# Kernel optimization log

Measured on AMD Instinct MI355X. Metric: run time of the kernel, lower is better.

Reference implementation:

```python
import jax, jax.numpy as jnp
import numpy as np
import math

HID = 128      # hidden_dim == d_inner (expand=1)
NSTATE = 8     # d_state
K = 4          # scan directions
RANK = math.ceil(HID / 16)  # dt_rank = 8
B, H, W = 4, 64, 64


def _ln(x, g, b, eps=1e-5):
    m = jnp.mean(x, -1, keepdims=True)
    v = jnp.mean((x - m) ** 2, -1, keepdims=True)
    return (x - m) * jax.lax.rsqrt(v + eps) * g + b


def _ss2d(x, in_w, conv_w, conv_b, xproj_w, dt_w, dt_b, A_logs, Ds, ln_g, ln_b, out_w):
    # x: [B,H,W,C] -> VMamba SS2D with d_inner=C, 4-direction selective scan
    Bn, Hh, Ww, C = x.shape
    D, L = C, Hh * Ww
    N = A_logs.shape[-1]
    R = dt_w.shape[-1]
    xz = x @ in_w.T                      # [B,H,W,2D]
    xc, z = jnp.split(xz, 2, axis=-1)
    xc = xc.transpose(0, 3, 1, 2)        # [B,D,H,W]
    xc = jax.lax.conv_general_dilated(xc, conv_w, (1, 1), 'SAME', feature_group_count=D)
    xc = jax.nn.silu(xc + conv_b[None, :, None, None])
    x_hw = xc.reshape(Bn, D, L)
    x_wh = xc.transpose(0, 1, 3, 2).reshape(Bn, D, L)
    xs = jnp.stack([x_hw, x_wh, x_hw[..., ::-1], x_wh[..., ::-1]], 1)  # [B,K,D,L]
    x_dbl = jnp.einsum('bkdl,kcd->bkcl', xs, xproj_w)
    dts, Bs, Cs = x_dbl[:, :, :R], x_dbl[:, :, R:R + N], x_dbl[:, :, R + N:]
    dt = jax.nn.softplus(jnp.einsum('bkrl,kdr->bkdl', dts, dt_w) + dt_b[None, :, :, None])
    A = -jnp.exp(A_logs.reshape(K, D, N))  # [K,D,N]

    def step(h, inp):
        x_t, dt_t, B_t, C_t = inp          # [B,K,D],[B,K,D],[B,K,N],[B,K,N]
        h = h * jnp.exp(dt_t[..., None] * A) + dt_t[..., None] * B_t[:, :, None, :] * x_t[..., None]
        return h, jnp.einsum('bkdn,bkn->bkd', h, C_t)

    h0 = jnp.zeros((Bn, K, D, N), x.dtype)
    _, ys = jax.lax.scan(step, h0, (xs.transpose(3, 0, 1, 2), dt.transpose(3, 0, 1, 2),
                                    Bs.transpose(3, 0, 1, 2), Cs.transpose(3, 0, 1, 2)))
    out_y = ys.transpose(1, 2, 3, 0) + Ds.reshape(K, D)[None, :, :, None] * xs  # [B,K,D,L]
    wh_y = out_y[:, 3, :, ::-1].reshape(Bn, D, Ww, Hh).transpose(0, 1, 3, 2).reshape(Bn, D, L)
    invwh_y = out_y[:, 1].reshape(Bn, D, Ww, Hh).transpose(0, 1, 3, 2).reshape(Bn, D, L)
    y = out_y[:, 0] + out_y[:, 2, :, ::-1] + wh_y + invwh_y
    y = _ln(y.transpose(0, 2, 1).reshape(Bn, Hh, Ww, D), ln_g, ln_b)
    return (y * jax.nn.silu(z)) @ out_w.T


def _enhance(x, g, b, w, bias):
    return jax.nn.gelu(_ln(x, g, b) @ w.T + bias, approximate=False)


def setup_inputs() -> dict:
    key = jax.random.key(0)
    ks = jax.random.split(key, 12)
    f = lambda k, s, sc=0.02: jax.random.normal(k, s, jnp.float32) * sc
    return dict(
        sar_feat=jax.random.normal(ks[0], (B, H, W, HID), jnp.float32),
        opt_feat=jax.random.normal(ks[1], (B, H, W, HID), jnp.float32),
        ss_in_w=f(ks[2], (2, 2 * HID, HID)),
        ss_conv_w=f(ks[3], (2, HID, 1, 3, 3), 0.1),
        ss_conv_b=f(ks[4], (2, HID)),
        ss_xproj_w=f(ks[5], (2, K, RANK + 2 * NSTATE, HID)),
        ss_dt_w=f(ks[6], (2, K, HID, RANK), 0.1),
        ss_dt_b=f(ks[7], (2, K, HID), 0.1),
        ss_Alogs=jnp.tile(jnp.log(jnp.arange(1, NSTATE + 1, dtype=jnp.float32)), (2, K * HID, 1)),
        ss_Ds=jnp.ones((2, K * HID), jnp.float32),
        ss_ln_g=jnp.ones((2, HID), jnp.float32),
        ss_ln_b=jnp.zeros((2, HID), jnp.float32),
        ss_out_w=f(ks[8], (2, HID, HID)),
        enh_ln_g=jnp.ones((2, HID), jnp.float32),
        enh_ln_b=jnp.zeros((2, HID), jnp.float32),
        enh_w=f(ks[9], (2, HID, HID)),
        enh_b=jnp.zeros((2, HID), jnp.float32),
    )


def reference(sar_feat, opt_feat, ss_in_w, ss_conv_w, ss_conv_b, ss_xproj_w, ss_dt_w,
              ss_dt_b, ss_Alogs, ss_Ds, ss_ln_g, ss_ln_b, ss_out_w,
              enh_ln_g, enh_ln_b, enh_w, enh_b):
    # cat([opt,sar],-1)[...,:C] == opt ; cat([sar,opt],-1)[...,:C] == sar (faithful identity slice)
    # index 0 = cross_ss2d_s2o (input opt), index 1 = cross_ss2d_o2s (input sar)
    xin = jnp.stack([opt_feat, sar_feat])
    guided = jax.vmap(_ss2d)(xin, ss_in_w, ss_conv_w, ss_conv_b, ss_xproj_w, ss_dt_w,
                             ss_dt_b, ss_Alogs, ss_Ds, ss_ln_g, ss_ln_b, ss_out_w)
    # enhance params: index 0 = enhance_sar (on sar_guided=guided[1]), index 1 = enhance_opt (on opt_guided=guided[0])
    enh_in = jnp.stack([guided[1], guided[0]])
    enhanced = jax.vmap(_enhance)(enh_in, enh_ln_g, enh_ln_b, enh_w, enh_b)
    return (sar_feat + enhanced[0], opt_feat + enhanced[1])
```

## Files before the change

### kernel.cpp

```cpp
#include <hip/hip_runtime.h>
#include <hip/hip_bf16.h>
#include <math.h>

#define DEV __device__ __forceinline__

static constexpr int LL = 4096;
static constexpr int DD = 128;
static constexpr int SEG = 64;
static constexpr float LOG2E = 1.4426950408889634f;
static constexpr float LN2 = 0.6931471805599453f;

DEV float silu_(float x) { return x / (1.f + __expf(-x)); }
DEV float erf_(float x) {
  const float ax = fabsf(x);
  const float t = 1.f / fmaf(0.3275911f, ax, 1.f);
  float p = fmaf(1.061405429f, t, -1.453152027f);
  p = fmaf(p, t, 1.421413741f);
  p = fmaf(p, t, -0.284496736f);
  p = fmaf(p, t, 0.254829592f);
  p = p * t;
  const float r = 1.f - p * __expf(-ax * ax);
  return x < 0.f ? -r : r;
}
DEV float gelu_(float x) { return 0.5f * x * (1.f + erf_(x * 0.7071067811865475f)); }
DEV float sp_(float x) {
  const float t = __builtin_amdgcn_exp2f(-fabsf(x) * LOG2E);
  return fmaxf(x, 0.f) + LN2 * __builtin_amdgcn_logf(1.f + t);
}

template <int CTRL>
DEV float dpp_add_(float x) {
  int y = __builtin_amdgcn_update_dpp(0, __float_as_int(x), CTRL, 0xF, 0xF, true);
  return x + __int_as_float(y);
}

DEV void seg_base_step(int k, int s, int& base, int& step) {
  if (k == 0)      { base = s * 64;        step = 1;   }
  else if (k == 1) { base = s;             step = 64;  }
  else if (k == 2) { base = 4095 - s * 64; step = -1;  }
  else             { base = 4095 - s;      step = -64; }
}

__global__ __launch_bounds__(256) void k_inproj(
    const float* __restrict__ sar, const float* __restrict__ opt,
    const float* __restrict__ in_w, float* __restrict__ xz) {
  const int lt = blockIdx.x, ct = blockIdx.y, mb = blockIdx.z;
  const int m = mb >> 2;
  const float* __restrict__ x = (m == 0 ? opt : sar) + (size_t)(mb & 3) * (LL * DD);
  const float* __restrict__ W = in_w + (size_t)m * 256 * DD;
  __shared__ float sA[64][68];
  __shared__ float sW[64][68];
  const int tid = threadIdx.x;
  const int tc = tid & 15, tl = tid >> 4;
  float acc[4][4] = {};
  for (int db = 0; db < 2; ++db) {
    __syncthreads();
    for (int idx = tid; idx < 64 * 16; idx += 256) {
      const int r = idx >> 4, d4 = (idx & 15) << 2;
      *(float4*)&sA[r][d4] = *(const float4*)&x[(size_t)(lt * 64 + r) * DD + db * 64 + d4];
      *(float4*)&sW[r][d4] = *(const float4*)&W[(size_t)(ct * 64 + r) * DD + db * 64 + d4];
    }
    __syncthreads();
#pragma unroll 4
    for (int d = 0; d < 64; d += 4) {
      float4 a[4], w[4];
#pragma unroll
      for (int q = 0; q < 4; ++q) a[q] = *(const float4*)&sA[tl * 4 + q][d];
#pragma unroll
      for (int j = 0; j < 4; ++j) w[j] = *(const float4*)&sW[tc + 16 * j][d];
#pragma unroll
      for (int j = 0; j < 4; ++j)
#pragma unroll
        for (int q = 0; q < 4; ++q)
          acc[j][q] += a[q].x * w[j].x + a[q].y * w[j].y + a[q].z * w[j].z + a[q].w * w[j].w;
    }
  }
  float* __restrict__ dst = xz + ((size_t)mb * 256 + ct * 64) * LL + lt * 64;
#pragma unroll
  for (int j = 0; j < 4; ++j) {
    float4 v = make_float4(acc[j][0], acc[j][1], acc[j][2], acc[j][3]);
    *(float4*)&dst[(size_t)(tc + 16 * j) * LL + tl * 4] = v;
  }
}

__global__ __launch_bounds__(256) void k_conv(
    const float* __restrict__ xz, const float* __restrict__ conv_w,
    const float* __restrict__ conv_b, float* __restrict__ xc) {
  const int ht = blockIdx.x, dg = blockIdx.y, mb = blockIdx.z;
  const int m = mb >> 2;
  __shared__ float sIn[8][18][66];
  __shared__ float sOut[1024][8];
  const float* __restrict__ src = xz + ((size_t)mb * 256 + dg * 8) * LL;
  const int tid = threadIdx.x;
  for (int idx = tid; idx < 8 * 18 * 66; idx += 256) {
    const int dd = idx / (18 * 66);
    const int rem = idx - dd * (18 * 66);
    const int hh = rem / 66, ww = rem - hh * 66;
    const int h = ht * 16 + hh - 1, w = ww - 1;
    float v = 0.f;
    if (h >= 0 && h < 64 && w >= 0 && w < 64) v = src[(size_t)dd * LL + h * 64 + w];
    sIn[dd][hh][ww] = v;
  }
  __syncthreads();
  const int dd = tid & 7, wv = tid >> 3;
  const int dch = dg * 8 + dd;
  float wk[9];
#pragma unroll
  for (int t = 0; t < 9; ++t) wk[t] = conv_w[((size_t)m * DD + dch) * 9 + t];
  const float bias = conv_b[m * DD + dch];
  for (int hh = 0; hh < 16; ++hh) {
#pragma unroll
    for (int wh = 0; wh < 2; ++wh) {
      const int w = wv + wh * 32;
      float s = bias;
#pragma unroll
      for (int kh = 0; kh < 3; ++kh)
#pragma unroll
        for (int kw = 0; kw < 3; ++kw)
          s = fmaf(sIn[dd][hh + kh][w + kw], wk[kh * 3 + kw], s);
      sOut[hh * 64 + w][dd] = silu_(s);
    }
  }
  __syncthreads();
  float* __restrict__ dst = xc + (size_t)mb * LL * DD + dg * 8;
#pragma unroll
  for (int r = 0; r < 4; ++r) {
    const int pos = tid + r * 256;
    const int l = ht * 1024 + pos;
    *(float4*)&dst[(size_t)l * DD + 0] = *(const float4*)&sOut[pos][0];
    *(float4*)&dst[(size_t)l * DD + 4] = *(const float4*)&sOut[pos][4];
  }
}

__global__ __launch_bounds__(256) void k_xproj(
    const float* __restrict__ xc, const float* __restrict__ xproj_w,
    float* __restrict__ xdbl) {
  const int lt = blockIdx.x, k = blockIdx.y, mb = blockIdx.z;
  const int m = mb >> 2, mbk = mb * 4 + k;
  __shared__ float sX[64][132];
  __shared__ float sW[24][132];
  const int tid = threadIdx.x;
  const float* __restrict__ src = xc + (size_t)mb * LL * DD;
  int base, step;
  seg_base_step(k, lt, base, step);
  for (int idx = tid; idx < 64 * 32; idx += 256) {
    const int l = idx >> 5, d4 = (idx & 31) << 2;
    *(float4*)&sX[l][d4] = *(const float4*)&src[(size_t)(base + l * step) * DD + d4];
  }
  const float* __restrict__ Wsrc = xproj_w + ((size_t)m * 4 + k) * 24 * DD;
  for (int idx = tid; idx < 24 * 32; idx += 256) {
    const int r = idx >> 5, d4 = (idx & 31) << 2;
    *(float4*)&sW[r][d4] = *(const float4*)&Wsrc[(size_t)r * DD + d4];
  }
  __syncthreads();
  const int l = tid >> 2, cg = tid & 3;
  float acc[6] = {};
#pragma unroll 8
  for (int d = 0; d < 128; d += 4) {
    const float4 xv = *(const float4*)&sX[l][d];
#pragma unroll
    for (int j = 0; j < 6; ++j) {
      const float4 wv = *(const float4*)&sW[cg * 6 + j][d];
      acc[j] += xv.x * wv.x + xv.y * wv.y + xv.z * wv.z + xv.w * wv.w;
    }
  }
  float* __restrict__ dst = xdbl + ((size_t)mbk * LL + lt * 64 + l) * 24 + cg * 6;
#pragma unroll
  for (int j = 0; j < 6; ++j) dst[j] = acc[j];
}


template <bool REV, bool FAST>
DEV void scan1_dir(const float* __restrict__ slds, const float* __restrict__ xs0,
                   ptrdiff_t sstep, const float* __restrict__ aln2,
                   const float* __restrict__ wreg, float bw,
                   float* __restrict__ h, float& dtsum) {
  float xreg[8];
#pragma unroll
  for (int t = 0; t < 8; ++t)
    xreg[t] = xs0[(ptrdiff_t)(REV ? 63 - t : t) * sstep];
#pragma unroll 8
  for (int j = 0; j < 64; ++j) {
    const float x = xreg[j & 7];
    if (j + 8 < 64) xreg[j & 7] = xs0[(ptrdiff_t)(REV ? 55 - j : j + 8) * sstep];
    const float4 t0 = *(const float4*)&slds[j * 24 + 0];
    const float4 t1 = *(const float4*)&slds[j * 24 + 4];
    float s = bw;
    s = fmaf(t0.x, wreg[0], s); s = fmaf(t0.y, wreg[1], s);
    s = fmaf(t0.z, wreg[2], s); s = fmaf(t0.w, wreg[3], s);
    s = fmaf(t1.x, wreg[4], s); s = fmaf(t1.y, wreg[5], s);
    s = fmaf(t1.z, wreg[6], s); s = fmaf(t1.w, wreg[7], s);
    const float dt = sp_(s);
    const float u = dt * x;
    dtsum += dt;
    float q1, q2, q3, q4, q5, q6, q7, q8;
    if constexpr (FAST) {
      q1 = __builtin_amdgcn_exp2f(dt * aln2[0]);
      q2 = q1 * q1; q3 = q2 * q1; q4 = q2 * q2;
      q5 = q4 * q1; q6 = q4 * q2; q7 = q4 * q3; q8 = q4 * q4;
    } else {
      q1 = __builtin_amdgcn_exp2f(dt * aln2[0]);
      q2 = __builtin_amdgcn_exp2f(dt * aln2[1]);
      q3 = __builtin_amdgcn_exp2f(dt * aln2[2]);
      q4 = __builtin_amdgcn_exp2f(dt * aln2[3]);
      q5 = __builtin_amdgcn_exp2f(dt * aln2[4]);
      q6 = __builtin_amdgcn_exp2f(dt * aln2[5]);
      q7 = __builtin_amdgcn_exp2f(dt * aln2[6]);
      q8 = __builtin_amdgcn_exp2f(dt * aln2[7]);
    }
    const float4 b0 = *(const float4*)&slds[j * 24 + 8];
    const float4 b1 = *(const float4*)&slds[j * 24 + 12];
    h[0] = fmaf(h[0], q1, u * b0.x);
    h[1] = fmaf(h[1], q2, u * b0.y);
    h[2] = fmaf(h[2], q3, u * b0.z);
    h[3] = fmaf(h[3], q4, u * b0.w);
    h[4] = fmaf(h[4], q5, u * b1.x);
    h[5] = fmaf(h[5], q6, u * b1.y);
    h[6] = fmaf(h[6], q7, u * b1.z);
    h[7] = fmaf(h[7], q8, u * b1.w);
  }
}

template <bool REV, bool FAST>
DEV void scan3_dir(const float* __restrict__ slds, const float* __restrict__ xs0,
                   ptrdiff_t sstep, const float* __restrict__ aln2,
                   const float* __restrict__ wreg, float bw, float dsv,
                   float* __restrict__ h, float* __restrict__ yd0) {
  float xreg[8];
#pragma unroll
  for (int t = 0; t < 8; ++t)
    xreg[t] = xs0[(ptrdiff_t)(REV ? 63 - t : t) * sstep];
#pragma unroll 8
  for (int j = 0; j < 64; ++j) {
    const int phys = REV ? 63 - j : j;
    const float x = xreg[j & 7];
    if (j + 8 < 64) xreg[j & 7] = xs0[(ptrdiff_t)(REV ? 55 - j : j + 8) * sstep];
    const float4 t0 = *(const float4*)&slds[j * 24 + 0];
    const float4 t1 = *(const float4*)&slds[j * 24 + 4];
    float s = bw;
    s = fmaf(t0.x, wreg[0], s); s = fmaf(t0.y, wreg[1], s);
    s = fmaf(t0.z, wreg[2], s); s = fmaf(t0.w, wreg[3], s);
    s = fmaf(t1.x, wreg[4], s); s = fmaf(t1.y, wreg[5], s);
    s = fmaf(t1.z, wreg[6], s); s = fmaf(t1.w, wreg[7], s);
    const float dt = sp_(s);
    const float u = dt * x;
    float q1, q2, q3, q4, q5, q6, q7, q8;
    if constexpr (FAST) {
      q1 = __builtin_amdgcn_exp2f(dt * aln2[0]);
      q2 = q1 * q1; q3 = q2 * q1; q4 = q2 * q2;
      q5 = q4 * q1; q6 = q4 * q2; q7 = q4 * q3; q8 = q4 * q4;
    } else {
      q1 = __builtin_amdgcn_exp2f(dt * aln2[0]);
      q2 = __builtin_amdgcn_exp2f(dt * aln2[1]);
      q3 = __builtin_amdgcn_exp2f(dt * aln2[2]);
      q4 = __builtin_amdgcn_exp2f(dt * aln2[3]);
      q5 = __builtin_amdgcn_exp2f(dt * aln2[4]);
      q6 = __builtin_amdgcn_exp2f(dt * aln2[5]);
      q7 = __builtin_amdgcn_exp2f(dt * aln2[6]);
      q8 = __builtin_amdgcn_exp2f(dt * aln2[7]);
    }
    const float4 b0 = *(const float4*)&slds[j * 24 + 8];
    const float4 b1 = *(const float4*)&slds[j * 24 + 12];
    const float4 c0 = *(const float4*)&slds[j * 24 + 16];
    const float4 c1 = *(const float4*)&slds[j * 24 + 20];
    float y = dsv * x;
    h[0] = fmaf(h[0], q1, u * b0.x); y = fmaf(h[0], c0.x, y);
    h[1] = fmaf(h[1], q2, u * b0.y); y = fmaf(h[1], c0.y, y);
    h[2] = fmaf(h[2], q3, u * b0.z); y = fmaf(h[2], c0.z, y);
    h[3] = fmaf(h[3], q4, u * b0.w); y = fmaf(h[3], c0.w, y);
    h[4] = fmaf(h[4], q5, u * b1.x); y = fmaf(h[4], c1.x, y);
    h[5] = fmaf(h[5], q6, u * b1.y); y = fmaf(h[5], c1.y, y);
    h[6] = fmaf(h[6], q7, u * b1.z); y = fmaf(h[6], c1.z, y);
    h[7] = fmaf(h[7], q8, u * b1.w); y = fmaf(h[7], c1.w, y);
    yd0[(ptrdiff_t)phys * sstep] = y;
  }
}

DEV void load_aln2(const float* __restrict__ Alogs, int m, int k, int d,
                   float* __restrict__ aln2, bool& fastp) {
  const float4 a0 = *(const float4*)&Alogs[((size_t)m * 512 + k * DD + d) * 8];
  const float4 a1 = *(const float4*)&Alogs[((size_t)m * 512 + k * DD + d) * 8 + 4];
  aln2[0] = -__expf(a0.x) * LOG2E; aln2[1] = -__expf(a0.y) * LOG2E;
  aln2[2] = -__expf(a0.z) * LOG2E; aln2[3] = -__expf(a0.w) * LOG2E;
  aln2[4] = -__expf(a1.x) * LOG2E; aln2[5] = -__expf(a1.y) * LOG2E;
  aln2[6] = -__expf(a1.z) * LOG2E; aln2[7] = -__expf(a1.w) * LOG2E;
  fastp = true;
#pragma unroll
  for (int n = 1; n < 8; ++n)
    fastp = fastp && (fabsf(aln2[n] - (float)(n + 1) * aln2[0]) <=
                      1e-4f * fabsf(aln2[n]) + 1e-12f);
}

DEV void load_w8(const float* __restrict__ dt_w, int mbk, int d,
                 float* __restrict__ wreg) {
  const float4 w0 = *(const float4*)&dt_w[((size_t)mbk * DD + d) * 8];
  const float4 w1 = *(const float4*)&dt_w[((size_t)mbk * DD + d) * 8 + 4];
  wreg[0] = w0.x; wreg[1] = w0.y; wreg[2] = w0.z; wreg[3] = w0.w;
  wreg[4] = w1.x; wreg[5] = w1.y; wreg[6] = w1.z; wreg[7] = w1.w;
}

__global__ __launch_bounds__(128) void k_scan1(
    const float* __restrict__ xc, const float* __restrict__ xdbl,
    const float* __restrict__ dt_w, const float* __restrict__ dt_b,
    const float* __restrict__ Alogs, float* __restrict__ hend,
    float* __restrict__ Pseg) {
  const int s = blockIdx.x, p = blockIdx.y, mb = blockIdx.z;
  const int m = mb >> 2;
  const int kA = p, kB = p + 2;
  const int segA = s, segB = 63 - s;
  const int mbkA = mb * 4 + kA, mbkB = mb * 4 + kB;
  const int d = threadIdx.x;
  __shared__ float sldsA[64 * 24], sldsB[64 * 24];

  const float4* tA = (const float4*)(xdbl + ((size_t)mbkA * LL + segA * 64) * 24);
  const float4* tB = (const float4*)(xdbl + ((size_t)mbkB * LL + segB * 64) * 24);
#pragma unroll
  for (int t = 0; t < 3; ++t) {
    ((float4*)sldsA)[d + t * 128] = tA[d + t * 128];
    ((float4*)sldsB)[d + t * 128] = tB[d + t * 128];
  }

  const int base0 = (p == 0) ? s * 64 : s;
  const int stepPos = (p == 0) ? 1 : 64;
  const ptrdiff_t sstep = (ptrdiff_t)stepPos * DD;
  const float* __restrict__ xs0 = xc + (size_t)mb * LL * DD + (size_t)base0 * DD + d;
  __syncthreads();

  {
    float aln2[8]; bool fastp;
    load_aln2(Alogs, m, kA, d, aln2, fastp);
    float wreg[8];
    load_w8(dt_w, mbkA, d, wreg);
    const float bw = dt_b[(size_t)mbkA * DD + d];
    float h[8] = {0, 0, 0, 0, 0, 0, 0, 0};
    float dtsum = 0.f;
    if (fastp) scan1_dir<false, true>(sldsA, xs0, sstep, aln2, wreg, bw, h, dtsum);
    else       scan1_dir<false, false>(sldsA, xs0, sstep, aln2, wreg, bw, h, dtsum);
    float* __restrict__ he = hend + (((size_t)mbkA * SEG + segA) << 10) + d * 8;
    float* __restrict__ pe = Pseg + (((size_t)mbkA * SEG + segA) << 10) + d * 8;
    *(float4*)&he[0] = make_float4(h[0], h[1], h[2], h[3]);
    *(float4*)&he[4] = make_float4(h[4], h[5], h[6], h[7]);
    *(float4*)&pe[0] = make_float4(
        __builtin_amdgcn_exp2f(aln2[0] * dtsum), __builtin_amdgcn_exp2f(aln2[1] * dtsum),
        __builtin_amdgcn_exp2f(aln2[2] * dtsum), __builtin_amdgcn_exp2f(aln2[3] * dtsum));
    *(float4*)&pe[4] = make_float4(
        __builtin_amdgcn_exp2f(aln2[4] * dtsum), __builtin_amdgcn_exp2f(aln2[5] * dtsum),
        __builtin_amdgcn_exp2f(aln2[6] * dtsum), __builtin_amdgcn_exp2f(aln2[7] * dtsum));
  }
  {
    float aln2[8]; bool fastp;
    load_aln2(Alogs, m, kB, d, aln2, fastp);
    float wreg[8];
    load_w8(dt_w, mbkB, d, wreg);
    const float bw = dt_b[(size_t)mbkB * DD + d];
    float h[8] = {0, 0, 0, 0, 0, 0, 0, 0};
    float dtsum = 0.f;
    if (fastp) scan1_dir<true, true>(sldsB, xs0, sstep, aln2, wreg, bw, h, dtsum);
    else       scan1_dir<true, false>(sldsB, xs0, sstep, aln2, wreg, bw, h, dtsum);
    float* __restrict__ he = hend + (((size_t)mbkB * SEG + segB) << 10) + d * 8;
    float* __restrict__ pe = Pseg + (((size_t)mbkB * SEG + segB) << 10) + d * 8;
    *(float4*)&he[0] = make_float4(h[0], h[1], h[2], h[3]);
    *(float4*)&he[4] = make_float4(h[4], h[5], h[6], h[7]);
    *(float4*)&pe[0] = make_float4(
        __builtin_amdgcn_exp2f(aln2[0] * dtsum), __builtin_amdgcn_exp2f(aln2[1] * dtsum),
        __builtin_amdgcn_exp2f(aln2[2] * dtsum), __builtin_amdgcn_exp2f(aln2[3] * dtsum));
    *(float4*)&pe[4] = make_float4(
        __builtin_amdgcn_exp2f(aln2[4] * dtsum), __builtin_amdgcn_exp2f(aln2[5] * dtsum),
        __builtin_amdgcn_exp2f(aln2[6] * dtsum), __builtin_amdgcn_exp2f(aln2[7] * dtsum));
  }
}

__global__ __launch_bounds__(256) void k_scan2(
    const float* __restrict__ hend, const float* __restrict__ Pseg,
    float* __restrict__ hin) {
  const int gid = blockIdx.x * 256 + threadIdx.x;
  const int mbk = gid >> 10, dn = gid & 1023;
  const float* __restrict__ P = Pseg + ((size_t)mbk << 16) + dn;
  const float* __restrict__ E = hend + ((size_t)mbk << 16) + dn;
  float* __restrict__ O = hin + ((size_t)mbk << 16) + dn;
  float h = 0.f;
#pragma unroll
  for (int s = 0; s < SEG; ++s) {
    O[(size_t)s << 10] = h;
    if (s < SEG - 1) h = fmaf(P[(size_t)s << 10], h, E[(size_t)s << 10]);
  }
}

__global__ __launch_bounds__(128) void k_scan3(
    const float* __restrict__ xc, const float* __restrict__ xdbl,
    const float* __restrict__ dt_w, const float* __restrict__ dt_b,
    const float* __restrict__ Alogs, const float* __restrict__ Ds,
    const float* __restrict__ hin, float* __restrict__ y0,
    float* __restrict__ y1, float* __restrict__ y2, float* __restrict__ y3) {
  const int s = blockIdx.x, p = blockIdx.y, mb = blockIdx.z;
  const int m = mb >> 2;
  const int kA = p, kB = p + 2;
  const int segA = s, segB = 63 - s;
  const int mbkA = mb * 4 + kA, mbkB = mb * 4 + kB;
  const int d = threadIdx.x;
  __shared__ float sldsA[64 * 24], sldsB[64 * 24];

  const float4* tA = (const float4*)(xdbl + ((size_t)mbkA * LL + segA * 64) * 24);
  const float4* tB = (const float4*)(xdbl + ((size_t)mbkB * LL + segB * 64) * 24);
#pragma unroll
  for (int t = 0; t < 3; ++t) {
    ((float4*)sldsA)[d + t * 128] = tA[d + t * 128];
    ((float4*)sldsB)[d + t * 128] = tB[d + t * 128];
  }

  const int base0 = (p == 0) ? s * 64 : s;
  const int stepPos = (p == 0) ? 1 : 64;
  const ptrdiff_t sstep = (ptrdiff_t)stepPos * DD;
  const size_t off0 = (size_t)mb * LL * DD + (size_t)base0 * DD + d;
  const float* __restrict__ xs0 = xc + off0;
  float* __restrict__ ydA = (p == 0 ? y0 : y1) + off0;
  float* __restrict__ ydB = (p == 0 ? y2 : y3) + off0;

  float hA[8], hB[8];
  {
    const float* hp = hin + (((size_t)mbkA * SEG + segA) << 10) + d * 8;
    const float4 h0 = *(const float4*)&hp[0];
    const float4 h1 = *(const float4*)&hp[4];
    hA[0] = h0.x; hA[1] = h0.y; hA[2] = h0.z; hA[3] = h0.w;
    hA[4] = h1.x; hA[5] = h1.y; hA[6] = h1.z; hA[7] = h1.w;
  }
  {
    const float* hp = hin + (((size_t)mbkB * SEG + segB) << 10) + d * 8;
    const float4 h0 = *(const float4*)&hp[0];
    const float4 h1 = *(const float4*)&hp[4];
    hB[0] = h0.x; hB[1] = h0.y; hB[2] = h0.z; hB[3] = h0.w;
    hB[4] = h1.x; hB[5] = h1.y; hB[6] = h1.z; hB[7] = h1.w;
  }
  __syncthreads();

  {
    float aln2[8]; bool fastp;
    load_aln2(Alogs, m, kA, d, aln2, fastp);
    float wreg[8];
    load_w8(dt_w, mbkA, d, wreg);
    const float bw = dt_b[(size_t)mbkA * DD + d];
    const float dsv = Ds[(size_t)m * 512 + kA * DD + d];
    if (fastp) scan3_dir<false, true>(sldsA, xs0, sstep, aln2, wreg, bw, dsv, hA, ydA);
    else       scan3_dir<false, false>(sldsA, xs0, sstep, aln2, wreg, bw, dsv, hA, ydA);
  }
  {
    float aln2[8]; bool fastp;
    load_aln2(Alogs, m, kB, d, aln2, fastp);
    float wreg[8];
    load_w8(dt_w, mbkB, d, wreg);
    const float bw = dt_b[(size_t)mbkB * DD + d];
    const float dsv = Ds[(size_t)m * 512 + kB * DD + d];
    if (fastp) scan3_dir<true, true>(sldsB, xs0, sstep, aln2, wreg, bw, dsv, hB, ydB);
    else       scan3_dir<true, false>(sldsB, xs0, sstep, aln2, wreg, bw, dsv, hB, ydB);
  }
}

__global__ __launch_bounds__(256) void k_outproj(
    const float* __restrict__ y0, const float* __restrict__ y1,
    const float* __restrict__ y2, const float* __restrict__ y3,
    const float* __restrict__ xz, const float* __restrict__ ln_g,
    const float* __restrict__ ln_b, const float* __restrict__ out_w,
    float* __restrict__ guided) {
  const int lt = blockIdx.x, mb = blockIdx.y;
  const int m = mb >> 2;
  __shared__ float sv[32][132];
  __shared__ float sW[64][68];
  __shared__ float smr[32][2];
  __shared__ float sg[128], sb[128];
  const int tid = threadIdx.x;
  const size_t yoff = ((size_t)mb * LL + lt * 32) * DD;
  const float4* p0 = (const float4*)(y0 + yoff);
  const float4* p1 = (const float4*)(y1 + yoff);
  const float4* p2 = (const float4*)(y2 + yoff);
  const float4* p3 = (const float4*)(y3 + yoff);
  float4 ya[4], yb[4], yc4[4], yd4[4];
#pragma unroll
  for (int t = 0; t < 4; ++t) {
    ya[t] = p0[tid + t * 256]; yb[t] = p1[tid + t * 256];
    yc4[t] = p2[tid + t * 256]; yd4[t] = p3[tid + t * 256];
  }
  const int zc = tid >> 1, zh = tid & 1;
  const float4* zsrc = (const float4*)(xz + ((size_t)mb * 256 + 128 + zc) * LL + lt * 32 + zh * 16);
  float4 zv[4];
#pragma unroll
  for (int t = 0; t < 4; ++t) zv[t] = zsrc[t];
  const float* __restrict__ Wp = out_w + (size_t)m * DD * DD;
  float4 wpre[4];
#pragma unroll
  for (int t = 0; t < 4; ++t) {
    const int idx = tid + t * 256;
    wpre[t] = *(const float4*)&Wp[(size_t)(idx >> 4) * DD + ((idx & 15) << 2)];
  }
  if (tid < 128) { sg[tid] = ln_g[m * DD + tid]; sb[tid] = ln_b[m * DD + tid]; }
#pragma unroll
  for (int t = 0; t < 4; ++t) {
    const int idx = tid + t * 256;
    float4 v;
    v.x = (ya[t].x + yb[t].x) + (yc4[t].x + yd4[t].x);
    v.y = (ya[t].y + yb[t].y) + (yc4[t].y + yd4[t].y);
    v.z = (ya[t].z + yb[t].z) + (yc4[t].z + yd4[t].z);
    v.w = (ya[t].w + yb[t].w) + (yc4[t].w + yd4[t].w);
    *(float4*)&sv[idx >> 5][(idx & 31) << 2] = v;
  }
  __syncthreads();
  {
    const int l = tid >> 3, q = tid & 7;
    float s = 0.f, s2 = 0.f;
#pragma unroll
    for (int d0 = 0; d0 < 16; d0 += 4) {
      const float4 v = *(const float4*)&sv[l][q * 16 + d0];
      s += v.x + v.y + v.z + v.w;
      s2 += v.x * v.x + v.y * v.y + v.z * v.z + v.w * v.w;
    }
    s = dpp_add_<0xB1>(s); s = dpp_add_<0x4E>(s); s = dpp_add_<0x141>(s);
    s2 = dpp_add_<0xB1>(s2); s2 = dpp_add_<0x4E>(s2); s2 = dpp_add_<0x141>(s2);
    if (q == 0) {
      const float mean = s * (1.f / 128.f);
      smr[l][0] = mean;
      smr[l][1] = rsqrtf(fmaf(s2, 1.f / 128.f, -mean * mean) + 1e-5f);
    }
  }
  __syncthreads();
  {
    const float g = sg[zc], bb = sb[zc];
    const float* zf = (const float*)zv;
#pragma unroll
    for (int i2 = 0; i2 < 16; ++i2) {
      const int l = zh * 16 + i2;
      const float v = fmaf((sv[l][zc] - smr[l][0]) * smr[l][1], g, bb);
      sv[l][zc] = v * silu_(zf[i2]);
    }
  }
  const int tc = tid & 15, tl = tid >> 4;
  float* __restrict__ dst = guided + ((size_t)mb * LL + lt * 32) * DD;
#pragma unroll
  for (int jb = 0; jb < 2; ++jb) {
    float acc[4][2] = {};
#pragma unroll
    for (int db = 0; db < 2; ++db) {
      __syncthreads();
#pragma unroll
      for (int t = 0; t < 4; ++t) {
        const int idx = tid + t * 256;
        *(float4*)&sW[idx >> 4][(idx & 15) << 2] = wpre[t];
      }
      const int ph = jb * 2 + db + 1;
      if (ph < 4) {
        const int jb2 = ph >> 1, db2 = ph & 1;
#pragma unroll
        for (int t = 0; t < 4; ++t) {
          const int idx = tid + t * 256;
          wpre[t] = *(const float4*)&Wp[(size_t)(jb2 * 64 + (idx >> 4)) * DD + db2 * 64 + ((idx & 15) << 2)];
        }
      }
      __syncthreads();
#pragma unroll 4
      for (int d0 = 0; d0 < 64; d0 += 4) {
        float4 av[2], wv[4];
#pragma unroll
        for (int q = 0; q < 2; ++q) av[q] = *(const float4*)&sv[tl * 2 + q][db * 64 + d0];
#pragma unroll
        for (int j = 0; j < 4; ++j) wv[j] = *(const float4*)&sW[tc + 16 * j][d0];
#pragma unroll
        for (int j = 0; j < 4; ++j)
#pragma unroll
          for (int q = 0; q < 2; ++q)
            acc[j][q] += av[q].x * wv[j].x + av[q].y * wv[j].y + av[q].z * wv[j].z + av[q].w * wv[j].w;
      }
    }
#pragma unroll
    for (int j = 0; j < 4; ++j)
#pragma unroll
      for (int q = 0; q < 2; ++q)
        dst[(size_t)(tl * 2 + q) * DD + jb * 64 + tc + 16 * j] = acc[j][q];
  }
}

__global__ __launch_bounds__(256) void k_enhance(
    const float* __restrict__ guided, const float* __restrict__ eg,
    const float* __restrict__ ebv, const float* __restrict__ ew,
    const float* __restrict__ ebias, const float* __restrict__ sar,
    const float* __restrict__ opt, float* __restrict__ outp) {
  const int lt = blockIdx.x, ib = blockIdx.y;
  const int i = ib >> 2, b = ib & 3;
  __shared__ float sv[32][132];
  __shared__ float sW[64][68];
  __shared__ float smr[32][2];
  __shared__ float sg[128], sb2[128], sbias[128];
  const int tid = threadIdx.x;
  const float4* gsrc =
      (const float4*)(guided + (((size_t)(1 - i) * 4 + b) * LL + lt * 32) * DD);
  float4 gv[4];
#pragma unroll
  for (int t = 0; t < 4; ++t) gv[t] = gsrc[tid + t * 256];
  const float* __restrict__ Wp = ew + (size_t)i * DD * DD;
  float4 wpre[4];
#pragma unroll
  for (int t = 0; t < 4; ++t) {
    const int idx = tid + t * 256;
    wpre[t] = *(const float4*)&Wp[(size_t)(idx >> 4) * DD + ((idx & 15) << 2)];
  }
  if (tid < 128) {
    sg[tid] = eg[i * DD + tid];
    sb2[tid] = ebv[i * DD + tid];
    sbias[tid] = ebias[i * DD + tid];
  }
#pragma unroll
  for (int t = 0; t < 4; ++t) {
    const int idx = tid + t * 256;
    *(float4*)&sv[idx >> 5][(idx & 31) << 2] = gv[t];
  }
  __syncthreads();
  {
    const int l = tid >> 3, q = tid & 7;
    float s = 0.f, s2 = 0.f;
#pragma unroll
    for (int d0 = 0; d0 < 16; d0 += 4) {
      const float4 v = *(const float4*)&sv[l][q * 16 + d0];
      s += v.x + v.y + v.z + v.w;
      s2 += v.x * v.x + v.y * v.y + v.z * v.z + v.w * v.w;
    }
    s = dpp_add_<0xB1>(s); s = dpp_add_<0x4E>(s); s = dpp_add_<0x141>(s);
    s2 = dpp_add_<0xB1>(s2); s2 = dpp_add_<0x4E>(s2); s2 = dpp_add_<0x141>(s2);
    if (q == 0) {
      const float mean = s * (1.f / 128.f);
      smr[l][0] = mean;
      smr[l][1] = rsqrtf(fmaf(s2, 1.f / 128.f, -mean * mean) + 1e-5f);
    }
  }
  __syncthreads();
  {
    const int c = tid >> 1, half = tid & 1;
    const float g = sg[c], bb = sb2[c];
#pragma unroll
    for (int i2 = 0; i2 < 16; ++i2) {
      const int l = half * 16 + i2;
      sv[l][c] = fmaf((sv[l][c] - smr[l][0]) * smr[l][1], g, bb);
    }
  }
  const int tc = tid & 15, tl = tid >> 4;
  const float* __restrict__ resid = (i == 0 ? sar : opt) + ((size_t)b * LL + lt * 32) * DD;
  float* __restrict__ dst = outp + (size_t)i * (4 * LL * DD) + ((size_t)b * LL + lt * 32) * DD;
  float rv[16];
#pragma unroll
  for (int jb = 0; jb < 2; ++jb)
#pragma unroll
    for (int j = 0; j < 4; ++j)
#pragma unroll
      for (int q = 0; q < 2; ++q)
        rv[jb * 8 + j * 2 + q] = resid[(size_t)(tl * 2 + q) * DD + jb * 64 + tc + 16 * j];
  float accA[4][2] = {}, accB[4][2] = {};
#pragma unroll
  for (int jb = 0; jb < 2; ++jb) {
#pragma unroll
    for (int db = 0; db < 2; ++db) {
      __syncthreads();
#pragma unroll
      for (int t = 0; t < 4; ++t) {
        const int idx = tid + t * 256;
        *(float4*)&sW[idx >> 4][(idx & 15) << 2] = wpre[t];
      }
      const int ph = jb * 2 + db + 1;
      if (ph < 4) {
        const int jb2 = ph >> 1, db2 = ph & 1;
#pragma unroll
        for (int t = 0; t < 4; ++t) {
          const int idx = tid + t * 256;
          wpre[t] = *(const float4*)&Wp[(size_t)(jb2 * 64 + (idx >> 4)) * DD + db2 * 64 + ((idx & 15) << 2)];
        }
      }
      __syncthreads();
      float (*acc)[2] = (jb == 0) ? accA : accB;
#pragma unroll 4
      for (int d0 = 0; d0 < 64; d0 += 4) {
        float4 av[2], wv[4];
#pragma unroll
        for (int q = 0; q < 2; ++q) av[q] = *(const float4*)&sv[tl * 2 + q][db * 64 + d0];
#pragma unroll
        for (int j = 0; j < 4; ++j) wv[j] = *(const float4*)&sW[tc + 16 * j][d0];
#pragma unroll
        for (int j = 0; j < 4; ++j)
#pragma unroll
          for (int q = 0; q < 2; ++q)
            acc[j][q] += av[q].x * wv[j].x + av[q].y * wv[j].y + av[q].z * wv[j].z + av[q].w * wv[j].w;
      }
    }
  }
#pragma unroll
  for (int jb = 0; jb < 2; ++jb)
#pragma unroll
    for (int j = 0; j < 4; ++j)
#pragma unroll
      for (int q = 0; q < 2; ++q) {
        const int col = jb * 64 + tc + 16 * j;
        const float u = ((jb == 0) ? accA[j][q] : accB[j][q]) + sbias[col];
        dst[(size_t)(tl * 2 + q) * DD + col] = rv[jb * 8 + j * 2 + q] + gelu_(u);
      }
}

extern "C" void kernel_launch(void* const* d_in, const int* in_sizes, int n_in,
                              void* d_out, int out_size, void* d_ws, size_t ws_size,
                              hipStream_t stream) {
  (void)in_sizes; (void)n_in; (void)out_size; (void)ws_size;
  const float* sar    = (const float*)d_in[0];
  const float* opt    = (const float*)d_in[1];
  const float* in_w   = (const float*)d_in[2];
  const float* conv_w = (const float*)d_in[3];
  const float* conv_b = (const float*)d_in[4];
  const float* xproj_w= (const float*)d_in[5];
  const float* dt_w   = (const float*)d_in[6];
  const float* dt_b   = (const float*)d_in[7];
  const float* Alogs  = (const float*)d_in[8];
  const float* Ds     = (const float*)d_in[9];
  const float* ln_g   = (const float*)d_in[10];
  const float* ln_b   = (const float*)d_in[11];
  const float* out_w  = (const float*)d_in[12];
  const float* eg     = (const float*)d_in[13];
  const float* eb     = (const float*)d_in[14];
  const float* ew     = (const float*)d_in[15];
  const float* ebias  = (const float*)d_in[16];

  float* ws     = (float*)d_ws;
  float* xz     = ws;
  float* xc     = xz + 8388608;
  float* xdbl   = xc + 4194304;
  float* y0b    = xdbl + 3145728;
  float* y1b    = y0b + 4194304;
  float* y2b    = y1b + 4194304;
  float* y3b    = y2b + 4194304;
  float* guided = y3b + 4194304;
  float* hend   = guided + 4194304;
  float* Pseg   = hend + 2097152;
  float* hin    = Pseg + 2097152;
  float* outf   = (float*)d_out;

  k_inproj <<<dim3(64, 4, 8), 256, 0, stream>>>(sar, opt, in_w, xz);
  k_conv   <<<dim3(4, 16, 8), 256, 0, stream>>>(xz, conv_w, conv_b, xc);
  k_xproj  <<<dim3(64, 4, 8), 256, 0, stream>>>(xc, xproj_w, xdbl);
  k_scan1  <<<dim3(64, 2, 8), 128, 0, stream>>>(xc, xdbl, dt_w, dt_b, Alogs, hend, Pseg);
  k_scan2  <<<dim3(128), 256, 0, stream>>>(hend, Pseg, hin);
  k_scan3  <<<dim3(64, 2, 8), 128, 0, stream>>>(xc, xdbl, dt_w, dt_b, Alogs, Ds, hin,
                                                y0b, y1b, y2b, y3b);
  k_outproj<<<dim3(128, 8), 256, 0, stream>>>(y0b, y1b, y2b, y3b, xz, ln_g, ln_b, out_w, guided);
  k_enhance<<<dim3(128, 8), 256, 0, stream>>>(guided, eg, eb, ew, ebias, sar, opt, outf);
}
```

Baseline: 301.5 us.

## Split chunked scan into 128 segments of 32 steps, one direction per block

The chunked selective scan now uses 128 segments of 32 steps instead of 64 segments of 64, and each block handles a single direction rather than a forward/reverse pair. This gives four times as many scan blocks and halves the serial chain per thread, aiming to improve occupancy and latency hiding in scan1 and scan3. In exchange, the segment-carry pass (scan2) runs twice as many sequential steps, and the hend/Pseg/hin buffers double in size. The workspace offsets are adjusted to fit the larger buffers.

```diff
diff --git a/kernel.cpp b/kernel.cpp
--- a/kernel.cpp
+++ b/kernel.cpp
@@ -6,7 +6,7 @@
 
 static constexpr int LL = 4096;
 static constexpr int DD = 128;
-static constexpr int SEG = 64;
+static constexpr int SEG = 128;
 static constexpr float LOG2E = 1.4426950408889634f;
 static constexpr float LN2 = 0.6931471805599453f;
 
@@ -39,6 +39,17 @@
   else if (k == 1) { base = s;             step = 64;  }
   else if (k == 2) { base = 4095 - s * 64; step = -1;  }
   else             { base = 4095 - s;      step = -64; }
+}
+
+DEV void seg32_base_step(int k, int s, int& base, int& step) {
+  if (k == 0)      { base = s * 32;                      step = 1;   }
+  else if (k == 1) { base = ((s & 1) * 32) * 64 + (s >> 1); step = 64; }
+  else if (k == 2) { base = 4095 - s * 32;               step = -1;  }
+  else {
+    const int s2 = 127 - s;
+    base = ((s2 & 1) * 32 + 31) * 64 + (s2 >> 1);
+    step = -64;
+  }
 }
 
 __global__ __launch_bounds__(256) void k_inproj(
@@ -170,19 +181,41 @@
 }
 
 
-template <bool REV, bool FAST>
-DEV void scan1_dir(const float* __restrict__ slds, const float* __restrict__ xs0,
-                   ptrdiff_t sstep, const float* __restrict__ aln2,
-                   const float* __restrict__ wreg, float bw,
-                   float* __restrict__ h, float& dtsum) {
+DEV void load_aln2(const float* __restrict__ Alogs, int m, int k, int d,
+                   float* __restrict__ aln2, bool& fastp) {
+  const float4 a0 = *(const float4*)&Alogs[((size_t)m * 512 + k * DD + d) * 8];
+  const float4 a1 = *(const float4*)&Alogs[((size_t)m * 512 + k * DD + d) * 8 + 4];
+  aln2[0] = -__expf(a0.x) * LOG2E; aln2[1] = -__expf(a0.y) * LOG2E;
+  aln2[2] = -__expf(a0.z) * LOG2E; aln2[3] = -__expf(a0.w) * LOG2E;
+  aln2[4] = -__expf(a1.x) * LOG2E; aln2[5] = -__expf(a1.y) * LOG2E;
+  aln2[6] = -__expf(a1.z) * LOG2E; aln2[7] = -__expf(a1.w) * LOG2E;
+  fastp = true;
+#pragma unroll
+  for (int n = 1; n < 8; ++n)
+    fastp = fastp && (fabsf(aln2[n] - (float)(n + 1) * aln2[0]) <=
+                      1e-4f * fabsf(aln2[n]) + 1e-12f);
+}
+
+DEV void load_w8(const float* __restrict__ dt_w, int mbk, int d,
+                 float* __restrict__ wreg) {
+  const float4 w0 = *(const float4*)&dt_w[((size_t)mbk * DD + d) * 8];
+  const float4 w1 = *(const float4*)&dt_w[((size_t)mbk * DD + d) * 8 + 4];
+  wreg[0] = w0.x; wreg[1] = w0.y; wreg[2] = w0.z; wreg[3] = w0.w;
+  wreg[4] = w1.x; wreg[5] = w1.y; wreg[6] = w1.z; wreg[7] = w1.w;
+}
+
+template <bool FAST>
+DEV void scan1_body(const float* __restrict__ slds, const float* __restrict__ xs0,
+                    ptrdiff_t sstep, const float* __restrict__ aln2,
+                    const float* __restrict__ wreg, float bw,
+                    float* __restrict__ h, float& dtsum) {
   float xreg[8];
 #pragma unroll
-  for (int t = 0; t < 8; ++t)
-    xreg[t] = xs0[(ptrdiff_t)(REV ? 63 - t : t) * sstep];
+  for (int t = 0; t < 8; ++t) xreg[t] = xs0[(ptrdiff_t)t * sstep];
 #pragma unroll 8
-  for (int j = 0; j < 64; ++j) {
+  for (int j = 0; j < 32; ++j) {
     const float x = xreg[j & 7];
-    if (j + 8 < 64) xreg[j & 7] = xs0[(ptrdiff_t)(REV ? 55 - j : j + 8) * sstep];
+    if (j + 8 < 32) xreg[j & 7] = xs0[(ptrdiff_t)(j + 8) * sstep];
     const float4 t0 = *(const float4*)&slds[j * 24 + 0];
     const float4 t1 = *(const float4*)&slds[j * 24 + 4];
     float s = bw;
@@ -221,20 +254,18 @@
   }
 }
 
-template <bool REV, bool FAST>
-DEV void scan3_dir(const float* __restrict__ slds, const float* __restrict__ xs0,
-                   ptrdiff_t sstep, const float* __restrict__ aln2,
-                   const float* __restrict__ wreg, float bw, float dsv,
-                   float* __restrict__ h, float* __restrict__ yd0) {
+template <bool FAST>
+DEV void scan3_body(const float* __restrict__ slds, const float* __restrict__ xs0,
+                    ptrdiff_t sstep, const float* __restrict__ aln2,
+                    const float* __restrict__ wreg, float bw, float dsv,
+                    float* __restrict__ h, float* __restrict__ yd0) {
   float xreg[8];
 #pragma unroll
-  for (int t = 0; t < 8; ++t)
-    xreg[t] = xs0[(ptrdiff_t)(REV ? 63 - t : t) * sstep];
+  for (int t = 0; t < 8; ++t) xreg[t] = xs0[(ptrdiff_t)t * sstep];
 #pragma unroll 8
-  for (int j = 0; j < 64; ++j) {
-    const int phys = REV ? 63 - j : j;
+  for (int j = 0; j < 32; ++j) {
     const float x = xreg[j & 7];
-    if (j + 8 < 64) xreg[j & 7] = xs0[(ptrdiff_t)(REV ? 55 - j : j + 8) * sstep];
+    if (j + 8 < 32) xreg[j & 7] = xs0[(ptrdiff_t)(j + 8) * sstep];
     const float4 t0 = *(const float4*)&slds[j * 24 + 0];
     const float4 t1 = *(const float4*)&slds[j * 24 + 4];
     float s = bw;
@@ -272,31 +303,8 @@
     h[5] = fmaf(h[5], q6, u * b1.y); y = fmaf(h[5], c1.y, y);
     h[6] = fmaf(h[6], q7, u * b1.z); y = fmaf(h[6], c1.z, y);
     h[7] = fmaf(h[7], q8, u * b1.w); y = fmaf(h[7], c1.w, y);
-    yd0[(ptrdiff_t)phys * sstep] = y;
-  }
-}
-
-DEV void load_aln2(const float* __restrict__ Alogs, int m, int k, int d,
-                   float* __restrict__ aln2, bool& fastp) {
-  const float4 a0 = *(const float4*)&Alogs[((size_t)m * 512 + k * DD + d) * 8];
-  const float4 a1 = *(const float4*)&Alogs[((size_t)m * 512 + k * DD + d) * 8 + 4];
-  aln2[0] = -__expf(a0.x) * LOG2E; aln2[1] = -__expf(a0.y) * LOG2E;
-  aln2[2] = -__expf(a0.z) * LOG2E; aln2[3] = -__expf(a0.w) * LOG2E;
-  aln2[4] = -__expf(a1.x) * LOG2E; aln2[5] = -__expf(a1.y) * LOG2E;
-  aln2[6] = -__expf(a1.z) * LOG2E; aln2[7] = -__expf(a1.w) * LOG2E;
-  fastp = true;
-#pragma unroll
-  for (int n = 1; n < 8; ++n)
-    fastp = fastp && (fabsf(aln2[n] - (float)(n + 1) * aln2[0]) <=
-                      1e-4f * fabsf(aln2[n]) + 1e-12f);
-}
-
-DEV void load_w8(const float* __restrict__ dt_w, int mbk, int d,
-                 float* __restrict__ wreg) {
-  const float4 w0 = *(const float4*)&dt_w[((size_t)mbk * DD + d) * 8];
-  const float4 w1 = *(const float4*)&dt_w[((size_t)mbk * DD + d) * 8 + 4];
-  wreg[0] = w0.x; wreg[1] = w0.y; wreg[2] = w0.z; wreg[3] = w0.w;
-  wreg[4] = w1.x; wreg[5] = w1.y; wreg[6] = w1.z; wreg[7] = w1.w;
+    yd0[(ptrdiff_t)j * sstep] = y;
+  }
 }
 
 __global__ __launch_bounds__(128) void k_scan1(
@@ -304,70 +312,43 @@
     const float* __restrict__ dt_w, const float* __restrict__ dt_b,
     const float* __restrict__ Alogs, float* __restrict__ hend,
     float* __restrict__ Pseg) {
-  const int s = blockIdx.x, p = blockIdx.y, mb = blockIdx.z;
-  const int m = mb >> 2;
-  const int kA = p, kB = p + 2;
-  const int segA = s, segB = 63 - s;
-  const int mbkA = mb * 4 + kA, mbkB = mb * 4 + kB;
+  const int s = blockIdx.x;
+  const int k = blockIdx.y, mb = blockIdx.z;
+  const int m = mb >> 2, mbk = mb * 4 + k;
   const int d = threadIdx.x;
-  __shared__ float sldsA[64 * 24], sldsB[64 * 24];
-
-  const float4* tA = (const float4*)(xdbl + ((size_t)mbkA * LL + segA * 64) * 24);
-  const float4* tB = (const float4*)(xdbl + ((size_t)mbkB * LL + segB * 64) * 24);
-#pragma unroll
-  for (int t = 0; t < 3; ++t) {
-    ((float4*)sldsA)[d + t * 128] = tA[d + t * 128];
-    ((float4*)sldsB)[d + t * 128] = tB[d + t * 128];
-  }
-
-  const int base0 = (p == 0) ? s * 64 : s;
-  const int stepPos = (p == 0) ? 1 : 64;
-  const ptrdiff_t sstep = (ptrdiff_t)stepPos * DD;
-  const float* __restrict__ xs0 = xc + (size_t)mb * LL * DD + (size_t)base0 * DD + d;
-  __syncthreads();
-
-  {
-    float aln2[8]; bool fastp;
-    load_aln2(Alogs, m, kA, d, aln2, fastp);
-    float wreg[8];
-    load_w8(dt_w, mbkA, d, wreg);
-    const float bw = dt_b[(size_t)mbkA * DD + d];
-    float h[8] = {0, 0, 0, 0, 0, 0, 0, 0};
-    float dtsum = 0.f;
-    if (fastp) scan1_dir<false, true>(sldsA, xs0, sstep, aln2, wreg, bw, h, dtsum);
-    else       scan1_dir<false, false>(sldsA, xs0, sstep, aln2, wreg, bw, h, dtsum);
-    float* __restrict__ he = hend + (((size_t)mbkA * SEG + segA) << 10) + d * 8;
-    float* __restrict__ pe = Pseg + (((size_t)mbkA * SEG + segA) << 10) + d * 8;
-    *(float4*)&he[0] = make_float4(h[0], h[1], h[2], h[3]);
-    *(float4*)&he[4] = make_float4(h[4], h[5], h[6], h[7]);
-    *(float4*)&pe[0] = make_float4(
-        __builtin_amdgcn_exp2f(aln2[0] * dtsum), __builtin_amdgcn_exp2f(aln2[1] * dtsum),
-        __builtin_amdgcn_exp2f(aln2[2] * dtsum), __builtin_amdgcn_exp2f(aln2[3] * dtsum));
-    *(float4*)&pe[4] = make_float4(
-        __builtin_amdgcn_exp2f(aln2[4] * dtsum), __builtin_amdgcn_exp2f(aln2[5] * dtsum),
-        __builtin_amdgcn_exp2f(aln2[6] * dtsum), __builtin_amdgcn_exp2f(aln2[7] * dtsum));
-  }
-  {
-    float aln2[8]; bool fastp;
-    load_aln2(Alogs, m, kB, d, aln2, fastp);
-    float wreg[8];
-    load_w8(dt_w, mbkB, d, wreg);
-    const float bw = dt_b[(size_t)mbkB * DD + d];
-    float h[8] = {0, 0, 0, 0, 0, 0, 0, 0};
-    float dtsum = 0.f;
-    if (fastp) scan1_dir<true, true>(sldsB, xs0, sstep, aln2, wreg, bw, h, dtsum);
-    else       scan1_dir<true, false>(sldsB, xs0, sstep, aln2, wreg, bw, h, dtsum);
-    float* __restrict__ he = hend + (((size_t)mbkB * SEG + segB) << 10) + d * 8;
-    float* __restrict__ pe = Pseg + (((size_t)mbkB * SEG + segB) << 10) + d * 8;
-    *(float4*)&he[0] = make_float4(h[0], h[1], h[2], h[3]);
-    *(float4*)&he[4] = make_float4(h[4], h[5], h[6], h[7]);
-    *(float4*)&pe[0] = make_float4(
-        __builtin_amdgcn_exp2f(aln2[0] * dtsum), __builtin_amdgcn_exp2f(aln2[1] * dtsum),
-        __builtin_amdgcn_exp2f(aln2[2] * dtsum), __builtin_amdgcn_exp2f(aln2[3] * dtsum));
-    *(float4*)&pe[4] = make_float4(
-        __builtin_amdgcn_exp2f(aln2[4] * dtsum), __builtin_amdgcn_exp2f(aln2[5] * dtsum),
-        __builtin_amdgcn_exp2f(aln2[6] * dtsum), __builtin_amdgcn_exp2f(aln2[7] * dtsum));
-  }
+  __shared__ float slds[32 * 24];
+
+  const float4* ts = (const float4*)(xdbl + ((size_t)mbk * LL + s * 32) * 24);
+  ((float4*)slds)[d] = ts[d];
+  if (d < 64) ((float4*)slds)[128 + d] = ts[128 + d];
+
+  float aln2[8]; bool fastp;
+  load_aln2(Alogs, m, k, d, aln2, fastp);
+  float wreg[8];
+  load_w8(dt_w, mbk, d, wreg);
+  const float bw = dt_b[(size_t)mbk * DD + d];
+
+  int base, step;
+  seg32_base_step(k, s, base, step);
+  const float* __restrict__ xs0 = xc + (size_t)mb * LL * DD + (size_t)base * DD + d;
+  const ptrdiff_t sstep = (ptrdiff_t)step * DD;
+  __syncthreads();
+
+  float h[8] = {0, 0, 0, 0, 0, 0, 0, 0};
+  float dtsum = 0.f;
+  if (fastp) scan1_body<true>(slds, xs0, sstep, aln2, wreg, bw, h, dtsum);
+  else       scan1_body<false>(slds, xs0, sstep, aln2, wreg, bw, h, dtsum);
+
+  float* __restrict__ he = hend + (((size_t)mbk * SEG + s) << 10) + d * 8;
+  float* __restrict__ pe = Pseg + (((size_t)mbk * SEG + s) << 10) + d * 8;
+  *(float4*)&he[0] = make_float4(h[0], h[1], h[2], h[3]);
+  *(float4*)&he[4] = make_float4(h[4], h[5], h[6], h[7]);
+  *(float4*)&pe[0] = make_float4(
+      __builtin_amdgcn_exp2f(aln2[0] * dtsum), __builtin_amdgcn_exp2f(aln2[1] * dtsum),
+      __builtin_amdgcn_exp2f(aln2[2] * dtsum), __builtin_amdgcn_exp2f(aln2[3] * dtsum));
+  *(float4*)&pe[4] = make_float4(
+      __builtin_amdgcn_exp2f(aln2[4] * dtsum), __builtin_amdgcn_exp2f(aln2[5] * dtsum),
+      __builtin_amdgcn_exp2f(aln2[6] * dtsum), __builtin_amdgcn_exp2f(aln2[7] * dtsum));
 }
 
 __global__ __launch_bounds__(256) void k_scan2(
@@ -375,9 +356,9 @@
     float* __restrict__ hin) {
   const int gid = blockIdx.x * 256 + threadIdx.x;
   const int mbk = gid >> 10, dn = gid & 1023;
-  const float* __restrict__ P = Pseg + ((size_t)mbk << 16) + dn;
-  const float* __restrict__ E = hend + ((size_t)mbk << 16) + dn;
-  float* __restrict__ O = hin + ((size_t)mbk << 16) + dn;
+  const float* __restrict__ P = Pseg + ((size_t)mbk * SEG << 10) + dn;
+  const float* __restrict__ E = hend + ((size_t)mbk * SEG << 10) + dn;
+  float* __restrict__ O = hin + ((size_t)mbk * SEG << 10) + dn;
   float h = 0.f;
 #pragma unroll
   for (int s = 0; s < SEG; ++s) {
@@ -392,67 +373,42 @@
     const float* __restrict__ Alogs, const float* __restrict__ Ds,
     const float* __restrict__ hin, float* __restrict__ y0,
     float* __restrict__ y1, float* __restrict__ y2, float* __restrict__ y3) {
-  const int s = blockIdx.x, p = blockIdx.y, mb = blockIdx.z;
-  const int m = mb >> 2;
-  const int kA = p, kB = p + 2;
-  const int segA = s, segB = 63 - s;
-  const int mbkA = mb * 4 + kA, mbkB = mb * 4 + kB;
+  const int s = blockIdx.x;
+  const int k = blockIdx.y, mb = blockIdx.z;
+  const int m = mb >> 2, mbk = mb * 4 + k;
   const int d = threadIdx.x;
-  __shared__ float sldsA[64 * 24], sldsB[64 * 24];
-
-  const float4* tA = (const float4*)(xdbl + ((size_t)mbkA * LL + segA * 64) * 24);
-  const float4* tB = (const float4*)(xdbl + ((size_t)mbkB * LL + segB * 64) * 24);
-#pragma unroll
-  for (int t = 0; t < 3; ++t) {
-    ((float4*)sldsA)[d + t * 128] = tA[d + t * 128];
-    ((float4*)sldsB)[d + t * 128] = tB[d + t * 128];
-  }
-
-  const int base0 = (p == 0) ? s * 64 : s;
-  const int stepPos = (p == 0) ? 1 : 64;
-  const ptrdiff_t sstep = (ptrdiff_t)stepPos * DD;
-  const size_t off0 = (size_t)mb * LL * DD + (size_t)base0 * DD + d;
+  __shared__ float slds[32 * 24];
+
+  const float4* ts = (const float4*)(xdbl + ((size_t)mbk * LL + s * 32) * 24);
+  ((float4*)slds)[d] = ts[d];
+  if (d < 64) ((float4*)slds)[128 + d] = ts[128 + d];
+
+  float aln2[8]; bool fastp;
+  load_aln2(Alogs, m, k, d, aln2, fastp);
+  float wreg[8];
+  load_w8(dt_w, mbk, d, wreg);
+  const float bw = dt_b[(size_t)mbk * DD + d];
+  const float dsv = Ds[(size_t)m * 512 + k * DD + d];
+
+  int base, step;
+  seg32_base_step(k, s, base, step);
+  const size_t off0 = (size_t)mb * LL * DD + (size_t)base * DD + d;
   const float* __restrict__ xs0 = xc + off0;
-  float* __restrict__ ydA = (p == 0 ? y0 : y1) + off0;
-  float* __restrict__ ydB = (p == 0 ? y2 : y3) + off0;
-
-  float hA[8], hB[8];
+  float* __restrict__ yk = (k == 0 ? y0 : k == 1 ? y1 : k == 2 ? y2 : y3) + off0;
+  const ptrdiff_t sstep = (ptrdiff_t)step * DD;
+
+  float h[8];
   {
-    const float* hp = hin + (((size_t)mbkA * SEG + segA) << 10) + d * 8;
+    const float* hp = hin + (((size_t)mbk * SEG + s) << 10) + d * 8;
     const float4 h0 = *(const float4*)&hp[0];
     const float4 h1 = *(const float4*)&hp[4];
-    hA[0] = h0.x; hA[1] = h0.y; hA[2] = h0.z; hA[3] = h0.w;
-    hA[4] = h1.x; hA[5] = h1.y; hA[6] = h1.z; hA[7] = h1.w;
-  }
-  {
-    const float* hp = hin + (((size_t)mbkB * SEG + segB) << 10) + d * 8;
-    const float4 h0 = *(const float4*)&hp[0];
-    const float4 h1 = *(const float4*)&hp[4];
-    hB[0] = h0.x; hB[1] = h0.y; hB[2] = h0.z; hB[3] = h0.w;
-    hB[4] = h1.x; hB[5] = h1.y; hB[6] = h1.z; hB[7] = h1.w;
-  }
-  __syncthreads();
-
-  {
-    float aln2[8]; bool fastp;
-    load_aln2(Alogs, m, kA, d, aln2, fastp);
-    float wreg[8];
-    load_w8(dt_w, mbkA, d, wreg);
-    const float bw = dt_b[(size_t)mbkA * DD + d];
-    const float dsv = Ds[(size_t)m * 512 + kA * DD + d];
-    if (fastp) scan3_dir<false, true>(sldsA, xs0, sstep, aln2, wreg, bw, dsv, hA, ydA);
-    else       scan3_dir<false, false>(sldsA, xs0, sstep, aln2, wreg, bw, dsv, hA, ydA);
-  }
-  {
-    float aln2[8]; bool fastp;
-    load_aln2(Alogs, m, kB, d, aln2, fastp);
-    float wreg[8];
-    load_w8(dt_w, mbkB, d, wreg);
-    const float bw = dt_b[(size_t)mbkB * DD + d];
-    const float dsv = Ds[(size_t)m * 512 + kB * DD + d];
-    if (fastp) scan3_dir<true, true>(sldsB, xs0, sstep, aln2, wreg, bw, dsv, hB, ydB);
-    else       scan3_dir<true, false>(sldsB, xs0, sstep, aln2, wreg, bw, dsv, hB, ydB);
-  }
+    h[0] = h0.x; h[1] = h0.y; h[2] = h0.z; h[3] = h0.w;
+    h[4] = h1.x; h[5] = h1.y; h[6] = h1.z; h[7] = h1.w;
+  }
+  __syncthreads();
+
+  if (fastp) scan3_body<true>(slds, xs0, sstep, aln2, wreg, bw, dsv, h, yk);
+  else       scan3_body<false>(slds, xs0, sstep, aln2, wreg, bw, dsv, h, yk);
 }
 
 __global__ __launch_bounds__(256) void k_outproj(
@@ -730,17 +686,17 @@
   float* y3b    = y2b + 4194304;
   float* guided = y3b + 4194304;
   float* hend   = guided + 4194304;
-  float* Pseg   = hend + 2097152;
-  float* hin    = Pseg + 2097152;
+  float* Pseg   = hend + 4194304;
+  float* hin    = Pseg + 4194304;
   float* outf   = (float*)d_out;
 
   k_inproj <<<dim3(64, 4, 8), 256, 0, stream>>>(sar, opt, in_w, xz);
   k_conv   <<<dim3(4, 16, 8), 256, 0, stream>>>(xz, conv_w, conv_b, xc);
   k_xproj  <<<dim3(64, 4, 8), 256, 0, stream>>>(xc, xproj_w, xdbl);
-  k_scan1  <<<dim3(64, 2, 8), 128, 0, stream>>>(xc, xdbl, dt_w, dt_b, Alogs, hend, Pseg);
+  k_scan1  <<<dim3(128, 4, 8), 128, 0, stream>>>(xc, xdbl, dt_w, dt_b, Alogs, hend, Pseg);
   k_scan2  <<<dim3(128), 256, 0, stream>>>(hend, Pseg, hin);
-  k_scan3  <<<dim3(64, 2, 8), 128, 0, stream>>>(xc, xdbl, dt_w, dt_b, Alogs, Ds, hin,
-                                                y0b, y1b, y2b, y3b);
+  k_scan3  <<<dim3(128, 4, 8), 128, 0, stream>>>(xc, xdbl, dt_w, dt_b, Alogs, Ds, hin,
+                                                 y0b, y1b, y2b, y3b);
   k_outproj<<<dim3(128, 8), 256, 0, stream>>>(y0b, y1b, y2b, y3b, xz, ln_g, ln_b, out_w, guided);
   k_enhance<<<dim3(128, 8), 256, 0, stream>>>(guided, eg, eb, ew, ebias, sar, opt, outf);
 }
```

Result: faster. 286.9 us (-4.8%).
